# Optimization experiments

Hardware: AMD Instinct MI355X
Metric: run time of the kernel (lower is better)

The kernel has to match this reference:

```python
import jax, jax.numpy as jnp
import numpy as np
from jax.scipy.special import gammaln

REG = 0.1  # reg_param from __init__


def setup_inputs() -> dict:
    key = jax.random.key(0)
    k1, k2 = jax.random.split(key)
    D, C, S, Q = 512, 64, 16, 2048  # feature_dim, n_way, shots, n_query
    X_support = jax.random.normal(k1, (C * S, D), dtype=jnp.float32)
    # balanced class labels (equivalent to argmax of a one-hot y)
    labels = jnp.arange(C * S, dtype=jnp.int32) % C
    X_query = jax.random.normal(k2, (Q, D), dtype=jnp.float32)
    # learned parameters, initialized exactly as in the torch module
    m = jnp.zeros((1, D), dtype=jnp.float32)
    kappa = jnp.asarray(0.1, dtype=jnp.float32)
    nu = jnp.asarray(float(D), dtype=jnp.float32)
    triu_diag = jnp.ones((D,), dtype=jnp.float32)
    triu_lower = jnp.eye(D, dtype=jnp.float32)
    return {"X_support": X_support, "labels": labels, "X_query": X_query,
            "m": m, "kappa": kappa, "nu": nu,
            "triu_diag": triu_diag, "triu_lower": triu_lower, "n_classes": 64}


def _forward(X_support, X_query, m, kappa, nu, triu_diag, triu_lower, labels, n_classes):
    N, D = X_support.shape
    C = int(n_classes)
    S = N // C  # balanced episode: N_j == S for every class

    # lower_triu = diag(|triu_diag|) + triu_lower * strictly_lower_mask
    mask = jnp.tril(jnp.ones((D, D), dtype=X_support.dtype), -1)
    L = jnp.diag(jnp.abs(triu_diag)) + triu_lower * mask

    kap = jnp.abs(kappa) + 1e-6
    nu_ = jnp.clip(nu, D - 1 + 1e-6)

    # group support samples by class: [C, S, D] (stable sort keeps per-class order)
    order = jnp.argsort(labels)
    Xg = X_support[order].reshape(C, S, D)
    Xmean = Xg.mean(axis=1)  # [C, D]

    # posterior means mu_j = kappa/(kappa+N) m + N/(kappa+N) mean(X_j)
    mu = (kap / (kap + S)) * m + (S / (kap + S)) * Xmean  # [C, D]

    # sum_outer(X_j) as one batched GEMM instead of a per-row loop
    XtX = jnp.einsum('csd,cse->cde', Xg, Xg)  # [C, D, D]
    base = L @ L.T + kap * (m.T @ m)          # [D, D], shared across classes
    S_ns = base[None] + XtX - (kap + S) * jnp.einsum('cd,ce->cde', mu, mu)
    sigma = S_ns * ((kap + S + 1.0) / ((nu_ + S - D + 1.0) * (kap + S)))  # [C, D, D]

    eye = jnp.eye(D, dtype=sigma.dtype)
    sigma_inv = (1.0 - REG) * jnp.linalg.inv(sigma) + REG * eye  # regularize()

    common = nu_ + S + 1.0 - D  # scalar (equal shots per class)
    _, logdet = jnp.linalg.slogdet(sigma)  # [C]
    bias = (gammaln(0.5 * (common + D)) - gammaln(0.5 * common)
            - 0.5 * D * jnp.log(common) - 0.5 * logdet)  # [C]

    # batched Mahalanobis distances: replaces nested python loops in predict()
    diff = X_query[None, :, :] - mu[:, None, :]              # [C, Q, D]
    t = jnp.einsum('cqd,cde->cqe', diff, sigma_inv)          # [C, Q, D]
    dist = jnp.sum(t * diff, axis=-1)                        # [C, Q]

    logits = bias[:, None] - 0.5 * (common + D) * jnp.log1p(dist / common)
    return logits.T  # [Q, C]


def reference(X_support, labels, X_query, m, kappa, nu, triu_diag, triu_lower, n_classes):
    return _forward(X_support, X_query, m, kappa, nu, triu_diag, triu_lower,
                    labels, n_classes)
```

## Files before the change

kernel.cpp:

```cpp
#include <hip/hip_runtime.h>
#include <math.h>

#define DD    512
#define CNUM  64
#define SHOTS 16
#define NSUP  1024
#define QNQ   2048
#define REGP  0.1f
#define XKS   4

typedef __attribute__((ext_vector_type(8))) short short8;
typedef __attribute__((ext_vector_type(4))) float f32x4;

__device__ __forceinline__ unsigned short f2bf(float f) {
  unsigned int u = __float_as_uint(f);
  unsigned int r = (u + 0x7fffu + ((u >> 16) & 1u)) >> 16;
  return (unsigned short)r;
}
__device__ __forceinline__ float bf2f(unsigned short h) {
  return __uint_as_float((unsigned int)h << 16);
}

static constexpr size_t OFF_W     = 0;
static constexpr size_t OFF_MU    = OFF_W     + 512*512;
static constexpr size_t OFF_Y     = OFF_MU    + 64*512;
static constexpr size_t OFF_Z     = OFF_Y     + 3136*512;
static constexpr size_t OFF_WM    = OFF_Z     + 3136;
static constexpr size_t OFF_CONST = OFF_WM    + 512;
static constexpr size_t OFF_IDX   = OFF_CONST + 16;
static constexpr size_t OFF_RMAP  = OFF_IDX   + 1024;
static constexpr size_t OFF_ZG    = OFF_RMAP  + 1088;
static constexpr size_t OFF_VMU   = OFF_ZG    + 1088;
static constexpr size_t OFF_MUBMU = OFF_VMU   + 1088;
static constexpr size_t OFF_MUN   = OFF_MUBMU + 64;
static constexpr size_t OFF_MINV  = OFF_MUN   + 64;
static constexpr size_t OFF_BIAS  = OFF_MINV  + 64*289;
static constexpr size_t OFF_QNRM  = OFF_BIAS  + 64;
static constexpr size_t OFF_YN    = OFF_QNRM  + 2048;
static constexpr size_t OFF_XMU   = OFF_YN    + 2048;
static constexpr size_t OFF_RG    = OFF_XMU   + (size_t)XKS*2048*64;
static constexpr size_t OFF_P     = OFF_RG    + 1088*2048;
static constexpr size_t OFF_PX    = OFF_P     + 3136*512;
static constexpr size_t OFF_PW    = OFF_PX    + 3136*512;


__device__ __forceinline__ void px_rows(const float* __restrict__ Xq,
    const float* __restrict__ Xs, unsigned short* __restrict__ PX, int r0) {
  int tid = threadIdx.x;
  int row = r0 + (tid >> 6), lane = tid & 63;
  const float* src = (row < QNQ) ? Xq + (size_t)row * DD
                                 : Xs + (size_t)(row - QNQ) * DD;
  size_t prow = (size_t)row * 1024;
  #pragma unroll
  for (int p = 0; p < 2; p++) {
    int col = lane * 8 + p * 4;
    float4 v = *(const float4*)(src + col);
    ushort4 hi, lo;
    hi.x = f2bf(v.x); lo.x = f2bf(v.x - bf2f(hi.x));
    hi.y = f2bf(v.y); lo.y = f2bf(v.y - bf2f(hi.y));
    hi.z = f2bf(v.z); lo.z = f2bf(v.z - bf2f(hi.z));
    hi.w = f2bf(v.w); lo.w = f2bf(v.w - bf2f(hi.w));
    *(ushort4*)(PX + prow + col) = hi;
    *(ushort4*)(PX + prow + 512 + col) = lo;
  }
}

__global__ __launch_bounds__(256) void f_init(const float* tdiag, const float* tlow,
    const float* kappa, const float* nu, const int* labels, const float* Xs,
    const float* Xq, const float* m, float* W, float* cst, int* idx,
    int* rowmap, float* mu, float* mun,
    unsigned short* PX, unsigned short* PW) {
  __shared__ float sh[2 * 64 * 68 + 32 * 33];
  __shared__ int sidx[SHOTS];
  int b = blockIdx.x, tid = threadIdx.x;
  if (b < 8) {
    int jb = b;
    float* Ld = sh;
    float* Wd = sh + 64 * 68;
    float* tsh = sh + 2 * 64 * 68;
    for (int t = tid; t < 4096; t += 256) {
      int r = t >> 6, c = t & 63;
      int gr = jb * 64 + r;
      float v = (r == c) ? fabsf(tdiag[gr])
              : (r > c ? tlow[(size_t)gr * DD + jb * 64 + c] : 0.0f);
      Ld[r * 68 + c] = v;
      Wd[r * 68 + c] = 0.0f;
    }
    __syncthreads();
    if (tid < 64) {
      int s = tid >> 4, t = tid & 15;
      int r0 = s * 16;
      #pragma unroll
      for (int i = 0; i < 16; i++) {
        float w = (i == t) ? 1.0f : 0.0f;
        #pragma unroll
        for (int k = 0; k < 16; k++)
          if (k < i) w -= Ld[(r0 + i) * 68 + r0 + k] * Wd[(r0 + k) * 68 + r0 + t];
        Wd[(r0 + i) * 68 + r0 + t] = w / Ld[(r0 + i) * 68 + r0 + i];
      }
    }
    __syncthreads();
    for (int g2 = 0; g2 < 2; g2++) {
      int r0 = g2 * 32 + 16, c0 = g2 * 32;
      int rr = tid >> 4, cc = tid & 15;
      float t_ = 0.0f;
      #pragma unroll
      for (int k = 0; k < 16; k++)
        t_ += Ld[(r0 + rr) * 68 + c0 + k] * Wd[(c0 + k) * 68 + c0 + cc];
      tsh[rr * 33 + cc] = t_;
      __syncthreads();
      float x = 0.0f;
      #pragma unroll
      for (int k = 0; k < 16; k++)
        x -= Wd[(r0 + rr) * 68 + r0 + k] * tsh[k * 33 + cc];
      Wd[(r0 + rr) * 68 + c0 + cc] = x;
      __syncthreads();
    }
    {
      int rr = tid >> 6, cc = tid & 63;
      #pragma unroll
      for (int p = 0; p < 4; p++) {
        int r = rr + p * 4, c = cc;
        if (c < 32) {
          float t_ = 0.0f;
          #pragma unroll
          for (int k = 0; k < 32; k++)
            t_ += Ld[(32 + r) * 68 + k] * Wd[k * 68 + c];
          tsh[r * 33 + c] = t_;
        } else {
          int c2 = c - 32;
          float t_ = 0.0f;
          #pragma unroll
          for (int k = 0; k < 32; k++)
            t_ += Ld[(32 + r + 16) * 68 + k] * Wd[k * 68 + c2];
          tsh[(r + 16) * 33 + c2] = t_;
        }
      }
      __syncthreads();
      #pragma unroll
      for (int p = 0; p < 4; p++) {
        int r = rr + p * 4, c = cc;
        int r2 = (c < 32) ? r : r + 16;
        int c2 = (c < 32) ? c : c - 32;
        float x = 0.0f;
        #pragma unroll
        for (int k = 0; k < 32; k++)
          x -= Wd[(32 + r2) * 68 + 32 + k] * tsh[k * 33 + c2];
        Wd[(32 + r2) * 68 + c2] = x;
      }
    }
    __syncthreads();
    float* Wblk = W + (size_t)(jb * 64) * DD + jb * 64;
    for (int t = tid; t < 4096; t += 256) {
      int r = t >> 6, c = t & 63;
      float v = Wd[r * 68 + c];
      Wblk[(size_t)r * DD + c] = v;
      unsigned short h = f2bf(v), l = f2bf(v - bf2f(h));
      size_t prow = (size_t)(jb * 64 + r) * 1024 + jb * 64 + c;
      PW[prow] = h;
      PW[prow + 512] = l;
    }
  } else if (b == 8) {
    if (tid == 0) {
      float kap = fabsf(kappa[0]) + 1e-6f;
      float nu_ = fmaxf(nu[0], (float)(DD - 1) + 1e-6f);
      float common = nu_ + (float)SHOTS + 1.0f - (float)DD;
      float scale = (kap + SHOTS + 1.0f) / ((nu_ + SHOTS - DD + 1.0f) * (kap + SHOTS));
      cst[0] = kap;
      cst[1] = scale;
      cst[2] = common;
      cst[3] = 0.5f * (common + DD);
      cst[4] = lgammaf(0.5f * (common + DD)) - lgammaf(0.5f * common)
               - 0.5f * (float)DD * logf(common);
      cst[5] = -(kap + SHOTS);
      cst[6] = kap / (kap + SHOTS);
      cst[7] = 1.0f / (kap + SHOTS);
      cst[8] = (float)DD * logf(scale);
      cst[9] = -1.0f / (kap + SHOTS);
    }
  } else if (b < 73) {
    int c = b - 9;
    if (tid < 64) {
      int lane = tid, cnt = 0;
      for (int i0 = 0; i0 < NSUP; i0 += 64) {
        int lab = labels[i0 + lane];
        unsigned long long mm = __ballot(lab == c);
        if (lab == c) {
          int pos = cnt + __popcll(mm & ((1ull << lane) - 1ull));
          if (pos < SHOTS) idx[c * SHOTS + pos] = i0 + lane;
        }
        cnt += __popcll(mm);
      }
    }
    __syncthreads();
    if (tid < 17)
      rowmap[c * 17 + tid] = (tid < SHOTS) ? (QNQ + idx[c * SHOTS + tid])
                                           : (QNQ + NSUP + c);
  } else {
    int c = b - 73;
    if (tid < 64) {
      int lane = tid, cnt = 0;
      for (int i0 = 0; i0 < NSUP; i0 += 64) {
        int lab = labels[i0 + lane];
        unsigned long long mm = __ballot(lab == c);
        if (lab == c) {
          int pos = cnt + __popcll(mm & ((1ull << lane) - 1ull));
          if (pos < SHOTS) sidx[pos] = i0 + lane;
        }
        cnt += __popcll(mm);
      }
    }
    __syncthreads();
    float kap = fabsf(kappa[0]) + 1e-6f;
    float cm = kap / (kap + SHOTS), cx = 1.0f / (kap + SHOTS);
    float* red = sh;
    float acc = 0.0f;
    size_t prow = (size_t)(3072 + c) * 1024;
    for (int d = tid; d < DD; d += 256) {
      float s = 0.0f;
      for (int sh_ = 0; sh_ < SHOTS; sh_++)
        s += Xs[(size_t)sidx[sh_] * DD + d];
      float v = cm * m[d] + cx * s;
      mu[(size_t)c * DD + d] = v;
      unsigned short h = f2bf(v), l = f2bf(v - bf2f(h));
      PX[prow + d] = h;
      PX[prow + 512 + d] = l;
      acc += v * v;
    }
    red[tid] = acc;
    __syncthreads();
    for (int off = 128; off > 0; off >>= 1) {
      if (tid < off) red[tid] += red[tid + off];
      __syncthreads();
    }
    if (tid == 0) mun[c] = red[0];
  }
}

__device__ __forceinline__ void tile_stage(float* S, const float* __restrict__ G, int ldg) {
  int tid = threadIdx.x;
  #pragma unroll
  for (int p = 0; p < 4; p++) {
    int f4 = tid + 256 * p;
    int row = f4 >> 4, c4 = (f4 & 15) * 4;
    *(float4*)&S[row * 68 + c4] = *(const float4*)(G + (size_t)row * ldg + c4);
  }
}
__device__ __forceinline__ void tile_fma(float acc[4][4], const float* As, const float* Bs) {
  int tid = threadIdx.x, tr = tid >> 4, tc = tid & 15;
  #pragma unroll
  for (int kk = 0; kk < 64; kk++) {
    float a[4];
    #pragma unroll
    for (int x = 0; x < 4; x++) a[x] = As[(tr * 4 + x) * 68 + kk];
    float4 bv = *(const float4*)&Bs[kk * 68 + tc * 4];
    float bb[4] = {bv.x, bv.y, bv.z, bv.w};
    #pragma unroll
    for (int x = 0; x < 4; x++)
      #pragma unroll
      for (int y = 0; y < 4; y++) acc[x][y] += a[x] * bb[y];
  }
}
__device__ __forceinline__ void tile_out_neg(const float acc[4][4], float* W,
    unsigned short* PW, int gr0, int gc0) {
  int tid = threadIdx.x, tr = tid >> 4, tc = tid & 15;
  #pragma unroll
  for (int x = 0; x < 4; x++) {
    #pragma unroll
    for (int y = 0; y < 4; y++) {
      float v = -acc[x][y];
      W[(size_t)(gr0 + tr * 4 + x) * DD + gc0 + tc * 4 + y] = v;
      unsigned short h = f2bf(v), l = f2bf(v - bf2f(h));
      size_t prow = (size_t)(gr0 + tr * 4 + x) * 1024 + gc0 + tc * 4 + y;
      PW[prow] = h;
      PW[prow + 512] = l;
    }
  }
}

#define GBK 16
__global__ __launch_bounds__(256) void k_m128_xmu(const float* __restrict__ tlow,
    const float* __restrict__ W_, float* __restrict__ Wout,
    const float* __restrict__ Xq, const float* __restrict__ Mu,
    float* __restrict__ xmup, unsigned short* __restrict__ PW) {
  __shared__ float sh[3 * 64 * 68];
  int b = blockIdx.x, tid = threadIdx.x;
  if (b < 4) {
    float* As = sh;
    float* Bs = sh + 64 * 68;
    float* tsh = sh + 2 * 64 * 68;
    int base = b * 128;
    float tacc[4][4] = {};
    tile_stage(As, tlow + (size_t)(base + 64) * DD + base, DD);
    tile_stage(Bs, W_ + (size_t)base * DD + base, DD);
    __syncthreads();
    tile_fma(tacc, As, Bs);
    __syncthreads();
    {
      int tr = tid >> 4, tc = tid & 15;
      #pragma unroll
      for (int x = 0; x < 4; x++)
        #pragma unroll
        for (int y = 0; y < 4; y++) tsh[(tr * 4 + x) * 68 + tc * 4 + y] = tacc[x][y];
    }
    tile_stage(As, W_ + (size_t)(base + 64) * DD + base + 64, DD);
    __syncthreads();
    float xacc[4][4] = {};
    tile_fma(xacc, As, tsh);
    tile_out_neg(xacc, Wout, PW, base + 64, base);
  } else {
    float* Ms = sh;
    float* Qs = sh + 64 * 68;
    int xb = b - 4;
    int bm = (xb & 63) * 32, kq = xb >> 6;
    int tr = tid >> 4, tc = tid & 15;
    float acc[4][2] = {};
    int k0s = kq * (DD / XKS), k0e = k0s + DD / XKS;
    for (int k0 = k0s; k0 < k0e; k0 += GBK) {
      {
        int row = tid >> 2, k4 = tid & 3;
        float4 v = *(const float4*)(Mu + (size_t)row * DD + k0 + k4 * 4);
        Ms[(k4 * 4 + 0) * 68 + row] = v.x; Ms[(k4 * 4 + 1) * 68 + row] = v.y;
        Ms[(k4 * 4 + 2) * 68 + row] = v.z; Ms[(k4 * 4 + 3) * 68 + row] = v.w;
      }
      if (tid < 128) {
        int row = tid >> 2, k4 = tid & 3;
        float4 v = *(const float4*)(Xq + (size_t)(bm + row) * DD + k0 + k4 * 4);
        Qs[(k4 * 4 + 0) * 36 + row] = v.x; Qs[(k4 * 4 + 1) * 36 + row] = v.y;
        Qs[(k4 * 4 + 2) * 36 + row] = v.z; Qs[(k4 * 4 + 3) * 36 + row] = v.w;
      }
      __syncthreads();
      #pragma unroll
      for (int kk = 0; kk < GBK; kk++) {
        float4 m0 = *(const float4*)&Ms[kk * 68 + tr * 4];
        float a[4] = {m0.x, m0.y, m0.z, m0.w};
        float q0 = Qs[kk * 36 + tc * 2], q1 = Qs[kk * 36 + tc * 2 + 1];
        #pragma unroll
        for (int y = 0; y < 4; y++) {
          acc[y][0] += a[y] * q0;
          acc[y][1] += a[y] * q1;
        }
      }
      __syncthreads();
    }
    #pragma unroll
    for (int y = 0; y < 4; y++) {
      float2 v = make_float2(acc[y][0], acc[y][1]);
      *(float2*)(xmup + ((size_t)kq * CNUM + tr * 4 + y) * QNQ + bm + tc * 2) = v;
    }
  }
}

__global__ __launch_bounds__(256) void k_m256(const float* __restrict__ tlow,
    float* __restrict__ W, unsigned short* __restrict__ PW,
    const float* __restrict__ Xq, const float* __restrict__ Xs,
    unsigned short* __restrict__ PX) {
  __shared__ float sh[3 * 64 * 68];
  int b = blockIdx.x, tid = threadIdx.x;
  if (b >= 8) { px_rows(Xq, Xs, PX, (b - 8) * 4); return; }
  float* As = sh;
  float* Bs = sh + 64 * 68;
  float* tsh = sh + 2 * 64 * 68;
  int g = b >> 2, rem = b & 3, i = rem >> 1, j = rem & 1;
  int base = g * 256;
  float xacc[4][4] = {};
  for (int k = 0; k <= i; k++) {
    float tacc[4][4] = {};
    for (int l = j; l < 2; l++) {
      __syncthreads();
      tile_stage(As, tlow + (size_t)(base + 128 + 64 * k) * DD + base + 64 * l, DD);
      tile_stage(Bs, W + (size_t)(base + 64 * l) * DD + base + 64 * j, DD);
      __syncthreads();
      tile_fma(tacc, As, Bs);
    }
    __syncthreads();
    {
      int tr = tid >> 4, tc = tid & 15;
      #pragma unroll
      for (int x = 0; x < 4; x++)
        #pragma unroll
        for (int y = 0; y < 4; y++) tsh[(tr * 4 + x) * 68 + tc * 4 + y] = tacc[x][y];
    }
    tile_stage(As, W + (size_t)(base + 128 + 64 * i) * DD + base + 128 + 64 * k, DD);
    __syncthreads();
    tile_fma(xacc, As, tsh);
  }
  tile_out_neg(xacc, W, PW, base + 128 + 64 * i, base + 64 * j);
}

__device__ __forceinline__ void nn64_sh(float* As, float* Bs,
    const float* __restrict__ A, int lda, const float* __restrict__ B, int ldb,
    float* __restrict__ Cd, int ldc, int k0, int k1, float sgn,
    unsigned short* __restrict__ Pw, int gr0, int gc0) {
  int tid = threadIdx.x, tr = tid >> 4, tc = tid & 15;
  float acc[4][4] = {};
  for (int kc = k0; kc < k1; kc += 64) {
    #pragma unroll
    for (int p = 0; p < 4; p++) {
      int f4 = tid + 256 * p;
      int row = f4 >> 4, c4 = f4 & 15;
      *(float4*)&As[row * 68 + c4 * 4] = *(const float4*)(A + (size_t)row * lda + kc + c4 * 4);
      *(float4*)&Bs[row * 68 + c4 * 4] = *(const float4*)(B + (size_t)(kc + row) * ldb + c4 * 4);
    }
    __syncthreads();
    #pragma unroll
    for (int kk = 0; kk < 64; kk++) {
      float a[4];
      #pragma unroll
      for (int x = 0; x < 4; x++) a[x] = As[(tr * 4 + x) * 68 + kk];
      float4 bv = *(const float4*)&Bs[kk * 68 + tc * 4];
      float bb[4] = {bv.x, bv.y, bv.z, bv.w};
      #pragma unroll
      for (int x = 0; x < 4; x++)
        #pragma unroll
        for (int y = 0; y < 4; y++) acc[x][y] += a[x] * bb[y];
    }
    __syncthreads();
  }
  #pragma unroll
  for (int x = 0; x < 4; x++) {
    float4 v = make_float4(sgn * acc[x][0], sgn * acc[x][1],
                           sgn * acc[x][2], sgn * acc[x][3]);
    *(float4*)(Cd + (size_t)(tr * 4 + x) * ldc + tc * 4) = v;
    if (Pw) {
      size_t prow = (size_t)(gr0 + tr * 4 + x) * 1024 + gc0 + tc * 4;
      float vv[4] = {v.x, v.y, v.z, v.w};
      #pragma unroll
      for (int y = 0; y < 4; y++) {
        unsigned short h = f2bf(vv[y]), l = f2bf(vv[y] - bf2f(h));
        Pw[prow + y] = h;
        Pw[prow + 512 + y] = l;
      }
    }
  }
}

__global__ __launch_bounds__(256) void k_triT(const float* __restrict__ tlow,
                                              const float* __restrict__ W,
                                              float* __restrict__ T,
                                              const float* __restrict__ Xq,
                                              const float* __restrict__ Xs,
                                              unsigned short* __restrict__ PX) {
  __shared__ float sh[2 * 64 * 68];
  int b = blockIdx.x;
  if (b >= 16) { px_rows(Xq, Xs, PX, 1024 + (b - 16) * 4); return; }
  int ti = b >> 2, tj = b & 3;
  const float* A = tlow + (size_t)(256 + ti * 64) * DD;
  const float* B = W + (size_t)tj * 64;
  float* Cd = T + (size_t)(ti * 64) * 256 + tj * 64;
  nn64_sh(sh, sh + 64 * 68, A, DD, B, DD, Cd, 256, tj * 64, 256, 1.0f, nullptr, 0, 0);
}

__global__ __launch_bounds__(256) void k_triX(float* __restrict__ W,
                                              const float* __restrict__ T,
                                              unsigned short* __restrict__ PW,
                                              const float* __restrict__ Xq,
                                              const float* __restrict__ Xs,
                                              unsigned short* __restrict__ PX) {
  __shared__ float sh[2 * 64 * 68];
  int b = blockIdx.x;
  if (b >= 16) { px_rows(Xq, Xs, PX, 2048 + (b - 16) * 4); return; }
  int ti = b >> 2, tj = b & 3;
  const float* A = W + (size_t)(256 + ti * 64) * DD + 256;
  const float* B = T + tj * 64;
  int gr0 = 256 + ti * 64, gc0 = tj * 64;
  float* Cd = W + (size_t)gr0 * DD + gc0;
  nn64_sh(sh, sh + 64 * 68, A, DD, B, 256, Cd, DD, 0, (ti + 1) * 64, -1.0f, PW, gr0, gc0);
}

#define PSTR 72
__global__ __launch_bounds__(256) void f_y_wm(const unsigned short* __restrict__ PX,
    const unsigned short* __restrict__ PW, const float* __restrict__ W,
    const float* __restrict__ m, float* __restrict__ Y,
    unsigned short* __restrict__ Pm, float* __restrict__ wm) {
  __shared__ unsigned short AshH[64 * PSTR];
  __shared__ unsigned short AshL[64 * PSTR];
  __shared__ unsigned short BshH[64 * PSTR];
  __shared__ unsigned short BshL[64 * PSTR];
  int b = blockIdx.x, tid = threadIdx.x;
  if (b < 392) {
    int mt = b >> 3, nt = b & 7;
    int bm = mt * 64, bn = nt * 64;
    int lane = tid & 63, wave = tid >> 6;
    int wr = wave >> 1, wc = wave & 1;
    int mrow = lane & 15, q = lane >> 4;
    f32x4 acc00 = {}, acc01 = {}, acc10 = {}, acc11 = {};
    int kchunks = nt + 1;
    for (int it = 0; it < kchunks; it++) {
      int kc = it * 64;
      #pragma unroll
      for (int p = 0; p < 2; p++) {
        int idx = tid + 256 * p;
        int row = idx >> 3, c8 = (idx & 7) * 8;
        *(short8*)&AshH[row * PSTR + c8] =
            *(const short8*)(PX + (size_t)(bm + row) * 1024 + kc + c8);
        *(short8*)&AshL[row * PSTR + c8] =
            *(const short8*)(PX + (size_t)(bm + row) * 1024 + 512 + kc + c8);
        *(short8*)&BshH[row * PSTR + c8] =
            *(const short8*)(PW + (size_t)(bn + row) * 1024 + kc + c8);
        *(short8*)&BshL[row * PSTR + c8] =
            *(const short8*)(PW + (size_t)(bn + row) * 1024 + 512 + kc + c8);
      }
      __syncthreads();
      #pragma unroll
      for (int ks = 0; ks < 2; ks++) {
        int ko = ks * 32 + q * 8;
        short8 ah0 = *(const short8*)&AshH[(wr * 32 + mrow) * PSTR + ko];
        short8 ah1 = *(const short8*)&AshH[(wr * 32 + 16 + mrow) * PSTR + ko];
        short8 al0 = *(const short8*)&AshL[(wr * 32 + mrow) * PSTR + ko];
        short8 al1 = *(const short8*)&AshL[(wr * 32 + 16 + mrow) * PSTR + ko];
        short8 bh0 = *(const short8*)&BshH[(wc * 32 + mrow) * PSTR + ko];
        short8 bh1 = *(const short8*)&BshH[(wc * 32 + 16 + mrow) * PSTR + ko];
        short8 bl0 = *(const short8*)&BshL[(wc * 32 + mrow) * PSTR + ko];
        short8 bl1 = *(const short8*)&BshL[(wc * 32 + 16 + mrow) * PSTR + ko];
        acc00 = __builtin_amdgcn_mfma_f32_16x16x32_bf16(ah0, bh0, acc00, 0, 0, 0);
        acc00 = __builtin_amdgcn_mfma_f32_16x16x32_bf16(ah0, bl0, acc00, 0, 0, 0);
        acc00 = __builtin_amdgcn_mfma_f32_16x16x32_bf16(al0, bh0, acc00, 0, 0, 0);
        acc01 = __builtin_amdgcn_mfma_f32_16x16x32_bf16(ah0, bh1, acc01, 0, 0, 0);
        acc01 = __builtin_amdgcn_mfma_f32_16x16x32_bf16(ah0, bl1, acc01, 0, 0, 0);
        acc01 = __builtin_amdgcn_mfma_f32_16x16x32_bf16(al0, bh1, acc01, 0, 0, 0);
        acc10 = __builtin_amdgcn_mfma_f32_16x16x32_bf16(ah1, bh0, acc10, 0, 0, 0);
        acc10 = __builtin_amdgcn_mfma_f32_16x16x32_bf16(ah1, bl0, acc10, 0, 0, 0);
        acc10 = __builtin_amdgcn_mfma_f32_16x16x32_bf16(al1, bh0, acc10, 0, 0, 0);
        acc11 = __builtin_amdgcn_mfma_f32_16x16x32_bf16(ah1, bh1, acc11, 0, 0, 0);
        acc11 = __builtin_amdgcn_mfma_f32_16x16x32_bf16(ah1, bl1, acc11, 0, 0, 0);
        acc11 = __builtin_amdgcn_mfma_f32_16x16x32_bf16(al1, bh1, acc11, 0, 0, 0);
      }
      __syncthreads();
    }
    #pragma unroll
    for (int r = 0; r < 4; r++) {
      int row0 = bm + wr * 32 + q * 4 + r;
      int row1 = row0 + 16;
      int col0 = bn + wc * 32 + mrow;
      float vv[4] = {acc00[r], acc01[r], acc10[r], acc11[r]};
      int rows[4] = {row0, row0, row1, row1};
      int cols[4] = {col0, col0 + 16, col0, col0 + 16};
      #pragma unroll
      for (int e = 0; e < 4; e++) {
        Y[(size_t)rows[e] * DD + cols[e]] = vv[e];
        unsigned short h = f2bf(vv[e]), l = f2bf(vv[e] - bf2f(h));
        Pm[(size_t)rows[e] * 1024 + cols[e]] = h;
        Pm[(size_t)rows[e] * 1024 + 512 + cols[e]] = l;
      }
    }
  } else {
    int wave = tid >> 6, lane = tid & 63;
    int row = (b - 392) * 4 + wave;
    float s = 0.0f;
    for (int j = lane; j <= row; j += 64) s += W[(size_t)row * DD + j] * m[j];
    for (int off = 32; off > 0; off >>= 1) s += __shfl_down(s, off);
    if (lane == 0) wm[row] = s;
  }
}

__global__ __launch_bounds__(256) void f_z_rg_gram(const unsigned short* __restrict__ Pm,
    const float* __restrict__ Y, const float* __restrict__ tdiag,
    const int* __restrict__ rowmap, const float* __restrict__ Xq,
    const float* __restrict__ wm, float* __restrict__ cst,
    float* __restrict__ Rg,
    float* __restrict__ z, float* __restrict__ qn, float* __restrict__ yn,
    float* __restrict__ zg, float* __restrict__ Vmu, float* __restrict__ muBmu,
    float* __restrict__ Minv, float* __restrict__ bias) {
  __shared__ float sh[9216];
  __shared__ float csmS;
  int b = blockIdx.x, tid = threadIdx.x;
  if (b < 64) {
    int c = b;
    int lane = tid & 63, wave = tid >> 6;
    float* Ys  = sh;
    float* aug = sh + 8772;
    float* zsv = aug + 306;
    float kap = cst[0], cst9 = cst[9];
    for (int t = tid; t < 17 * 128; t += 256) {
      int r = t >> 7, col = t & 127;
      *(float4*)&Ys[r * 516 + col * 4] =
          *(const float4*)(Y + (size_t)rowmap[c * 17 + r] * DD + col * 4);
    }
    float ldb_r = 0.0f;
    if (wave == 0) {
      float aa = 0.0f, ll = 0.0f;
      for (int t = lane; t < DD; t += 64) {
        float w = wm[t]; aa += w * w;
        ll += logf(fabsf(tdiag[t]));
      }
      #pragma unroll
      for (int off = 32; off > 0; off >>= 1) {
        aa += __shfl_xor(aa, off);
        ll += __shfl_xor(ll, off);
      }
      ldb_r = 2.0f * ll + logf(1.0f + kap * aa);
      if (lane == 0) csmS = kap / (1.0f + kap * aa);
    }
    __syncthreads();
    if (wave > 0) {
      for (int a = wave - 1; a < 17; a += 3) {
        float s = 0.0f;
        for (int j = lane; j < 128; j += 64) {
          float4 yv = *(const float4*)&Ys[a * 516 + j * 4];
          float4 wv = *(const float4*)(wm + j * 4);
          s += yv.x * wv.x + yv.y * wv.y + yv.z * wv.z + yv.w * wv.w;
        }
        #pragma unroll
        for (int off = 32; off > 0; off >>= 1) s += __shfl_xor(s, off);
        if (lane == 0) zsv[a] = s;
      }
    }
    __syncthreads();
    float csm = csmS;
    for (int e = tid; e < 153; e += 256) {
      int a = (int)((sqrtf(8.0f * (float)e + 1.0f) - 1.0f) * 0.5f);
      while (((a + 1) * (a + 2)) / 2 <= e) a++;
      while ((a * (a + 1)) / 2 > e) a--;
      int bb = e - (a * (a + 1)) / 2;
      const float* ra = &Ys[a * 516];
      const float* rb = &Ys[bb * 516];
      float s = 0.0f;
      for (int k = 0; k < 128; k++) {
        float4 va = *(const float4*)&ra[k * 4];
        float4 vb = *(const float4*)&rb[k * 4];
        s += va.x * vb.x + va.y * vb.y + va.z * vb.z + va.w * vb.w;
      }
      float g = s - csm * zsv[a] * zsv[bb];
      if (a == bb) g += (a < 16) ? 1.0f : cst9;
      aug[a * 18 + bb] = g;
      if (a != bb) aug[bb * 18 + a] = g;
    }
    __syncthreads();
    if (wave == 0) {
      float colv[17];
      bool left = lane < 17;
      bool right = (lane >= 17 && lane < 34);
      #pragma unroll
      for (int r = 0; r < 17; r++) {
        float lv = aug[r * 18 + (lane & 31)];
        colv[r] = left ? lv : ((right && (lane - 17) == r) ? 1.0f : 0.0f);
      }
      float det = 0.0f;
      #pragma unroll
      for (int k = 0; k < 17; k++) {
        float best = fabsf(colv[k]); int bp = k;
        #pragma unroll
        for (int r = k + 1; r < 17; r++) {
          float v = fabsf(colv[r]);
          if (v > best) { best = v; bp = r; }
        }
        int p = __shfl(bp, k);
        float pv = colv[k];
        #pragma unroll
        for (int r = k + 1; r < 17; r++) pv = (p == r) ? colv[r] : pv;
        float oldk = colv[k];
        #pragma unroll
        for (int r = k + 1; r < 17; r++) colv[r] = (p == r) ? oldk : colv[r];
        colv[k] = pv;
        float piv = __shfl(pv, k);
        if (lane == 0) det += logf(fabsf(piv));
        float invp = 1.0f / piv;
        float rk = pv * invp;
        colv[k] = rk;
        #pragma unroll
        for (int r = 0; r < 17; r++) {
          if (r == k) continue;
          float ck = __shfl(colv[r], k);
          colv[r] = fmaf(-ck, rk, colv[r]);
        }
      }
      if (right) {
        int bb = lane - 17;
        #pragma unroll
        for (int r = 0; r < 17; r++)
          Minv[(size_t)c * 289 + r * 17 + bb] = colv[r];
      }
      if (lane == 0) {
        float slog = logf(fabsf(cst[5])) + det;
        float logdetSigma = cst[8] + ldb_r + slog;
        bias[c] = cst[4] - 0.5f * logdetSigma;
      }
    } else if (wave == 1) {
      if (lane < 17) {
        float gv = aug[lane * 18 + 16];
        if (lane == 16) gv -= cst9;
        Vmu[c * 17 + lane] = gv;
        if (lane == 16) muBmu[c] = gv;
        zg[c * 17 + lane] = zsv[lane];
      }
    }
  } else if (b == 64) {
    if (tid < 64) {
      float aa = 0.0f, ll = 0.0f;
      for (int t = tid; t < DD; t += 64) {
        float w = wm[t]; aa += w * w;
        ll += logf(fabsf(tdiag[t]));
      }
      #pragma unroll
      for (int off = 32; off > 0; off >>= 1) {
        aa += __shfl_xor(aa, off);
        ll += __shfl_xor(ll, off);
      }
      if (tid == 0) {
        float kap = cst[0];
        cst[10] = kap / (1.0f + kap * aa);
        cst[11] = 2.0f * ll + logf(1.0f + kap * aa);
      }
    }
  } else if (b < 609) {
    unsigned short* ush = (unsigned short*)sh;
    unsigned short* AH = ush;
    unsigned short* AL = ush + 64 * PSTR;
    unsigned short* BH = ush + 2 * 64 * PSTR;
    unsigned short* BL = ush + 3 * 64 * PSTR;
    int rb = b - 65;
    int bm = (rb >> 5) * 64, bn = (rb & 31) * 64;
    int lane = tid & 63, wave = tid >> 6;
    int wr = wave >> 1, wc = wave & 1;
    int mrow = lane & 15, q = lane >> 4;
    int srowA[2];
    #pragma unroll
    for (int p = 0; p < 2; p++) srowA[p] = rowmap[bm + ((tid + 256 * p) >> 3)];
    f32x4 acc00 = {}, acc01 = {}, acc10 = {}, acc11 = {};
    for (int it = 0; it < 8; it++) {
      int kc = it * 64;
      #pragma unroll
      for (int p = 0; p < 2; p++) {
        int idx = tid + 256 * p;
        int row = idx >> 3, c8 = (idx & 7) * 8;
        *(short8*)&AH[row * PSTR + c8] =
            *(const short8*)(Pm + (size_t)srowA[p] * 1024 + kc + c8);
        *(short8*)&AL[row * PSTR + c8] =
            *(const short8*)(Pm + (size_t)srowA[p] * 1024 + 512 + kc + c8);
        *(short8*)&BH[row * PSTR + c8] =
            *(const short8*)(Pm + (size_t)(bn + row) * 1024 + kc + c8);
        *(short8*)&BL[row * PSTR + c8] =
            *(const short8*)(Pm + (size_t)(bn + row) * 1024 + 512 + kc + c8);
      }
      __syncthreads();
      #pragma unroll
      for (int ks = 0; ks < 2; ks++) {
        int ko = ks * 32 + q * 8;
        short8 ah0 = *(const short8*)&AH[(wr * 32 + mrow) * PSTR + ko];
        short8 ah1 = *(const short8*)&AH[(wr * 32 + 16 + mrow) * PSTR + ko];
        short8 al0 = *(const short8*)&AL[(wr * 32 + mrow) * PSTR + ko];
        short8 al1 = *(const short8*)&AL[(wr * 32 + 16 + mrow) * PSTR + ko];
        short8 bh0 = *(const short8*)&BH[(wc * 32 + mrow) * PSTR + ko];
        short8 bh1 = *(const short8*)&BH[(wc * 32 + 16 + mrow) * PSTR + ko];
        short8 bl0 = *(const short8*)&BL[(wc * 32 + mrow) * PSTR + ko];
        short8 bl1 = *(const short8*)&BL[(wc * 32 + 16 + mrow) * PSTR + ko];
        acc00 = __builtin_amdgcn_mfma_f32_16x16x32_bf16(ah0, bh0, acc00, 0, 0, 0);
        acc00 = __builtin_amdgcn_mfma_f32_16x16x32_bf16(ah0, bl0, acc00, 0, 0, 0);
        acc00 = __builtin_amdgcn_mfma_f32_16x16x32_bf16(al0, bh0, acc00, 0, 0, 0);
        acc01 = __builtin_amdgcn_mfma_f32_16x16x32_bf16(ah0, bh1, acc01, 0, 0, 0);
        acc01 = __builtin_amdgcn_mfma_f32_16x16x32_bf16(ah0, bl1, acc01, 0, 0, 0);
        acc01 = __builtin_amdgcn_mfma_f32_16x16x32_bf16(al0, bh1, acc01, 0, 0, 0);
        acc10 = __builtin_amdgcn_mfma_f32_16x16x32_bf16(ah1, bh0, acc10, 0, 0, 0);
        acc10 = __builtin_amdgcn_mfma_f32_16x16x32_bf16(ah1, bl0, acc10, 0, 0, 0);
        acc10 = __builtin_amdgcn_mfma_f32_16x16x32_bf16(al1, bh0, acc10, 0, 0, 0);
        acc11 = __builtin_amdgcn_mfma_f32_16x16x32_bf16(ah1, bh1, acc11, 0, 0, 0);
        acc11 = __builtin_amdgcn_mfma_f32_16x16x32_bf16(ah1, bl1, acc11, 0, 0, 0);
        acc11 = __builtin_amdgcn_mfma_f32_16x16x32_bf16(al1, bh1, acc11, 0, 0, 0);
      }
      __syncthreads();
    }
    #pragma unroll
    for (int r = 0; r < 4; r++) {
      int row0 = bm + wr * 32 + q * 4 + r;
      int row1 = row0 + 16;
      int col0 = bn + wc * 32 + mrow;
      Rg[(size_t)row0 * QNQ + col0]      = acc00[r];
      Rg[(size_t)row0 * QNQ + col0 + 16] = acc01[r];
      Rg[(size_t)row1 * QNQ + col0]      = acc10[r];
      Rg[(size_t)row1 * QNQ + col0 + 16] = acc11[r];
    }
  } else {
    int wave = tid >> 6, lane = tid & 63;
    int row = (b - 609) * 4 + wave;
    const float* xr = Xq + (size_t)row * DD;
    const float* yr = Y + (size_t)row * DD;
    float sz = 0.0f, s1 = 0.0f, s2 = 0.0f;
    for (int j4 = lane; j4 < 128; j4 += 64) {
      float4 xv = *(const float4*)(xr + j4 * 4);
      float4 yv = *(const float4*)(yr + j4 * 4);
      float4 wv = *(const float4*)(wm + j4 * 4);
      sz += yv.x * wv.x + yv.y * wv.y + yv.z * wv.z + yv.w * wv.w;
      s1 += xv.x * xv.x + xv.y * xv.y + xv.z * xv.z + xv.w * xv.w;
      s2 += yv.x * yv.x + yv.y * yv.y + yv.z * yv.z + yv.w * yv.w;
    }
    for (int off = 32; off > 0; off >>= 1) {
      sz += __shfl_down(sz, off);
      s1 += __shfl_down(s1, off);
      s2 += __shfl_down(s2, off);
    }
    if (lane == 0) {
      z[row] = sz;
      qn[row] = s1;
      yn[row] = s2;
    }
  }
}

__global__ __launch_bounds__(256) void k_logits(const float* __restrict__ Rg,
    const float* z, const float* zg,
    const float* Vmu, const float* muBmu, const float* mun, const float* yn,
    const float* qn, const float* xmup, const float* Minv, const float* bias,
    const float* cst, float* out) {
  __shared__ float Ms[289], Vs[17], Zs[17];
  int c = blockIdx.y;
  int q = blockIdx.x * 256 + threadIdx.x;
  for (int t = threadIdx.x; t < 289; t += 256) Ms[t] = Minv[(size_t)c * 289 + t];
  if (threadIdx.x < 17) {
    Vs[threadIdx.x] = Vmu[c * 17 + threadIdx.x];
    Zs[threadIdx.x] = zg[c * 17 + threadIdx.x];
  }
  __syncthreads();
  float csm = cst[10], scale = cst[1], common = cst[2], coef = cst[3];
  float zq = z[q];
  float r[17];
  float xBmu = 0.0f;
  for (int a = 0; a < 17; a++) {
    float raw = Rg[(size_t)(c * 17 + a) * QNQ + q] - csm * Zs[a] * zq;
    if (a == 16) xBmu = raw;
    r[a] = raw - Vs[a];
  }
  float qB = yn[q] - csm * zq * zq;
  float quadB = qB - 2.0f * xBmu + muBmu[c];
  float corr = 0.0f;
  for (int a = 0; a < 17; a++) {
    float e = 0.0f;
    for (int bb = 0; bb < 17; bb++) e += Ms[a * 17 + bb] * r[bb];
    corr += r[a] * e;
  }
  float distB = (quadB - corr) / scale;
  float xm = 0.0f;
  #pragma unroll
  for (int p = 0; p < XKS; p++)
    xm += xmup[((size_t)(p * CNUM + c)) * QNQ + q];
  float dn = qn[q] - 2.0f * xm + mun[c];
  float dist = (1.0f - REGP) * distB + REGP * dn;
  out[(size_t)q * CNUM + c] = bias[c] - coef * log1pf(dist / common);
}

extern "C" void kernel_launch(void* const* d_in, const int* in_sizes, int n_in,
                              void* d_out, int out_size, void* d_ws, size_t ws_size,
                              hipStream_t stream) {
  const float* Xs    = (const float*)d_in[0];
  const int*   labels= (const int*)d_in[1];
  const float* Xq    = (const float*)d_in[2];
  const float* m     = (const float*)d_in[3];
  const float* kappa = (const float*)d_in[4];
  const float* nu    = (const float*)d_in[5];
  const float* tdiag = (const float*)d_in[6];
  const float* tlow  = (const float*)d_in[7];
  float* ws = (float*)d_ws;
  float* W    = ws + OFF_W;
  float* mu   = ws + OFF_MU;
  float* Y    = ws + OFF_Y;
  float* z    = ws + OFF_Z;
  float* wm   = ws + OFF_WM;
  float* cst  = ws + OFF_CONST;
  int*   idx  = (int*)(ws + OFF_IDX);
  int*   rmap = (int*)(ws + OFF_RMAP);
  float* zg   = ws + OFF_ZG;
  float* Vmu  = ws + OFF_VMU;
  float* muBmu= ws + OFF_MUBMU;
  float* mun  = ws + OFF_MUN;
  float* Minv = ws + OFF_MINV;
  float* bias = ws + OFF_BIAS;
  float* qn   = ws + OFF_QNRM;
  float* yn   = ws + OFF_YN;
  float* xmup = ws + OFF_XMU;
  float* Rg   = ws + OFF_RG;
  unsigned short* P  = (unsigned short*)(ws + OFF_P);
  unsigned short* PX = (unsigned short*)(ws + OFF_PX);
  unsigned short* PW = (unsigned short*)(ws + OFF_PW);
  float* Ttmp = ws + OFF_RG;
  float* out  = (float*)d_out;

  f_init<<<137, 256, 0, stream>>>(tdiag, tlow, kappa, nu, labels, Xs, Xq, m,
                                  W, cst, idx, rmap, mu, mun, PX, PW);
  k_m128_xmu<<<260, 256, 0, stream>>>(tlow, W, W, Xq, mu, xmup, PW);
  k_m256<<<8 + 256, 256, 0, stream>>>(tlow, W, PW, Xq, Xs, PX);
  k_triT<<<16 + 256, 256, 0, stream>>>(tlow, W, Ttmp, Xq, Xs, PX);
  k_triX<<<16 + 256, 256, 0, stream>>>(W, Ttmp, PW, Xq, Xs, PX);
  f_y_wm<<<520, 256, 0, stream>>>(PX, PW, W, m, Y, P, wm);
  f_z_rg_gram<<<64 + 1 + 544 + 512, 256, 0, stream>>>(P, Y, tdiag, rmap, Xq, wm,
                                                      cst, Rg, z, qn, yn,
                                                      zg, Vmu, muBmu, Minv, bias);
  k_logits<<<dim3(QNQ / 256, CNUM), 256, 0, stream>>>(Rg, z, zg, Vmu, muBmu,
                                                      mun, yn, qn, xmup, Minv, bias,
                                                      cst, out);
  (void)in_sizes; (void)n_in; (void)out_size; (void)ws_size;
}
```

Baseline: 187.5 us.

## Merge label-index blocks, keep triangular inverse in registers, widen k-tile, batch rows

The rowmap computation moves into the mu blocks, which drops 64 redundant f_init blocks and the idx workspace buffer. The 16x16 diagonal-block triangular inverse now keeps its running column in registers instead of re-reading shared memory. The k_m128_xmu k-step doubles to 32 so each tile loads twice as much and there are fewer loop iterations and barriers. The row-norm blocks of f_z_rg_gram now handle two rows per wave, which halves their block count.

```diff
diff --git a/kernel.cpp b/kernel.cpp
--- a/kernel.cpp
+++ b/kernel.cpp
@@ -27,8 +27,7 @@
 static constexpr size_t OFF_Z     = OFF_Y     + 3136*512;
 static constexpr size_t OFF_WM    = OFF_Z     + 3136;
 static constexpr size_t OFF_CONST = OFF_WM    + 512;
-static constexpr size_t OFF_IDX   = OFF_CONST + 16;
-static constexpr size_t OFF_RMAP  = OFF_IDX   + 1024;
+static constexpr size_t OFF_RMAP  = OFF_CONST + 16;
 static constexpr size_t OFF_ZG    = OFF_RMAP  + 1088;
 static constexpr size_t OFF_VMU   = OFF_ZG    + 1088;
 static constexpr size_t OFF_MUBMU = OFF_VMU   + 1088;
@@ -67,7 +66,7 @@
 
 __global__ __launch_bounds__(256) void f_init(const float* tdiag, const float* tlow,
     const float* kappa, const float* nu, const int* labels, const float* Xs,
-    const float* Xq, const float* m, float* W, float* cst, int* idx,
+    const float* Xq, const float* m, float* W, float* cst,
     int* rowmap, float* mu, float* mun,
     unsigned short* PX, unsigned short* PW) {
   __shared__ float sh[2 * 64 * 68 + 32 * 33];
@@ -90,14 +89,17 @@
     if (tid < 64) {
       int s = tid >> 4, t = tid & 15;
       int r0 = s * 16;
+      float wreg[16];
       #pragma unroll
       for (int i = 0; i < 16; i++) {
         float w = (i == t) ? 1.0f : 0.0f;
         #pragma unroll
         for (int k = 0; k < 16; k++)
-          if (k < i) w -= Ld[(r0 + i) * 68 + r0 + k] * Wd[(r0 + k) * 68 + r0 + t];
-        Wd[(r0 + i) * 68 + r0 + t] = w / Ld[(r0 + i) * 68 + r0 + i];
-      }
+          if (k < i) w -= Ld[(r0 + i) * 68 + r0 + k] * wreg[k];
+        wreg[i] = w / Ld[(r0 + i) * 68 + r0 + i];
+      }
+      #pragma unroll
+      for (int i = 0; i < 16; i++) Wd[(r0 + i) * 68 + r0 + t] = wreg[i];
     }
     __syncthreads();
     for (int g2 = 0; g2 < 2; g2++) {
@@ -178,26 +180,8 @@
       cst[8] = (float)DD * logf(scale);
       cst[9] = -1.0f / (kap + SHOTS);
     }
-  } else if (b < 73) {
+  } else {
     int c = b - 9;
-    if (tid < 64) {
-      int lane = tid, cnt = 0;
-      for (int i0 = 0; i0 < NSUP; i0 += 64) {
-        int lab = labels[i0 + lane];
-        unsigned long long mm = __ballot(lab == c);
-        if (lab == c) {
-          int pos = cnt + __popcll(mm & ((1ull << lane) - 1ull));
-          if (pos < SHOTS) idx[c * SHOTS + pos] = i0 + lane;
-        }
-        cnt += __popcll(mm);
-      }
-    }
-    __syncthreads();
-    if (tid < 17)
-      rowmap[c * 17 + tid] = (tid < SHOTS) ? (QNQ + idx[c * SHOTS + tid])
-                                           : (QNQ + NSUP + c);
-  } else {
-    int c = b - 73;
     if (tid < 64) {
       int lane = tid, cnt = 0;
       for (int i0 = 0; i0 < NSUP; i0 += 64) {
@@ -211,6 +195,8 @@
       }
     }
     __syncthreads();
+    if (tid < 17)
+      rowmap[c * 17 + tid] = (tid < SHOTS) ? (QNQ + sidx[tid]) : (QNQ + NSUP + c);
     float kap = fabsf(kappa[0]) + 1e-6f;
     float cm = kap / (kap + SHOTS), cx = 1.0f / (kap + SHOTS);
     float* red = sh;
@@ -278,7 +264,7 @@
   }
 }
 
-#define GBK 16
+#define GBK 32
 __global__ __launch_bounds__(256) void k_m128_xmu(const float* __restrict__ tlow,
     const float* __restrict__ W_, float* __restrict__ Wout,
     const float* __restrict__ Xq, const float* __restrict__ Mu,
@@ -317,14 +303,16 @@
     float acc[4][2] = {};
     int k0s = kq * (DD / XKS), k0e = k0s + DD / XKS;
     for (int k0 = k0s; k0 < k0e; k0 += GBK) {
-      {
-        int row = tid >> 2, k4 = tid & 3;
+      #pragma unroll
+      for (int p = 0; p < 2; p++) {
+        int idx = tid + 256 * p;
+        int row = idx >> 3, k4 = idx & 7;
         float4 v = *(const float4*)(Mu + (size_t)row * DD + k0 + k4 * 4);
         Ms[(k4 * 4 + 0) * 68 + row] = v.x; Ms[(k4 * 4 + 1) * 68 + row] = v.y;
         Ms[(k4 * 4 + 2) * 68 + row] = v.z; Ms[(k4 * 4 + 3) * 68 + row] = v.w;
       }
-      if (tid < 128) {
-        int row = tid >> 2, k4 = tid & 3;
+      {
+        int row = tid >> 3, k4 = tid & 7;
         float4 v = *(const float4*)(Xq + (size_t)(bm + row) * DD + k0 + k4 * 4);
         Qs[(k4 * 4 + 0) * 36 + row] = v.x; Qs[(k4 * 4 + 1) * 36 + row] = v.y;
         Qs[(k4 * 4 + 2) * 36 + row] = v.z; Qs[(k4 * 4 + 3) * 36 + row] = v.w;
@@ -772,27 +760,31 @@
     }
   } else {
     int wave = tid >> 6, lane = tid & 63;
-    int row = (b - 609) * 4 + wave;
-    const float* xr = Xq + (size_t)row * DD;
-    const float* yr = Y + (size_t)row * DD;
-    float sz = 0.0f, s1 = 0.0f, s2 = 0.0f;
-    for (int j4 = lane; j4 < 128; j4 += 64) {
-      float4 xv = *(const float4*)(xr + j4 * 4);
-      float4 yv = *(const float4*)(yr + j4 * 4);
-      float4 wv = *(const float4*)(wm + j4 * 4);
-      sz += yv.x * wv.x + yv.y * wv.y + yv.z * wv.z + yv.w * wv.w;
-      s1 += xv.x * xv.x + xv.y * xv.y + xv.z * xv.z + xv.w * xv.w;
-      s2 += yv.x * yv.x + yv.y * yv.y + yv.z * yv.z + yv.w * yv.w;
-    }
-    for (int off = 32; off > 0; off >>= 1) {
-      sz += __shfl_down(sz, off);
-      s1 += __shfl_down(s1, off);
-      s2 += __shfl_down(s2, off);
-    }
-    if (lane == 0) {
-      z[row] = sz;
-      qn[row] = s1;
-      yn[row] = s2;
+    int base = (b - 609) * 8;
+    #pragma unroll
+    for (int rr = 0; rr < 2; rr++) {
+      int row = base + rr * 4 + wave;
+      const float* xr = Xq + (size_t)row * DD;
+      const float* yr = Y + (size_t)row * DD;
+      float sz = 0.0f, s1 = 0.0f, s2 = 0.0f;
+      for (int j4 = lane; j4 < 128; j4 += 64) {
+        float4 xv = *(const float4*)(xr + j4 * 4);
+        float4 yv = *(const float4*)(yr + j4 * 4);
+        float4 wv = *(const float4*)(wm + j4 * 4);
+        sz += yv.x * wv.x + yv.y * wv.y + yv.z * wv.z + yv.w * wv.w;
+        s1 += xv.x * xv.x + xv.y * xv.y + xv.z * xv.z + xv.w * xv.w;
+        s2 += yv.x * yv.x + yv.y * yv.y + yv.z * yv.z + yv.w * yv.w;
+      }
+      for (int off = 32; off > 0; off >>= 1) {
+        sz += __shfl_down(sz, off);
+        s1 += __shfl_down(s1, off);
+        s2 += __shfl_down(s2, off);
+      }
+      if (lane == 0) {
+        z[row] = sz;
+        qn[row] = s1;
+        yn[row] = s2;
+      }
     }
   }
 }
@@ -856,7 +848,6 @@
   float* z    = ws + OFF_Z;
   float* wm   = ws + OFF_WM;
   float* cst  = ws + OFF_CONST;
-  int*   idx  = (int*)(ws + OFF_IDX);
   int*   rmap = (int*)(ws + OFF_RMAP);
   float* zg   = ws + OFF_ZG;
   float* Vmu  = ws + OFF_VMU;
@@ -874,14 +865,14 @@
   float* Ttmp = ws + OFF_RG;
   float* out  = (float*)d_out;
 
-  f_init<<<137, 256, 0, stream>>>(tdiag, tlow, kappa, nu, labels, Xs, Xq, m,
-                                  W, cst, idx, rmap, mu, mun, PX, PW);
+  f_init<<<73, 256, 0, stream>>>(tdiag, tlow, kappa, nu, labels, Xs, Xq, m,
+                                 W, cst, rmap, mu, mun, PX, PW);
   k_m128_xmu<<<260, 256, 0, stream>>>(tlow, W, W, Xq, mu, xmup, PW);
   k_m256<<<8 + 256, 256, 0, stream>>>(tlow, W, PW, Xq, Xs, PX);
   k_triT<<<16 + 256, 256, 0, stream>>>(tlow, W, Ttmp, Xq, Xs, PX);
   k_triX<<<16 + 256, 256, 0, stream>>>(W, Ttmp, PW, Xq, Xs, PX);
   f_y_wm<<<520, 256, 0, stream>>>(PX, PW, W, m, Y, P, wm);
-  f_z_rg_gram<<<64 + 1 + 544 + 512, 256, 0, stream>>>(P, Y, tdiag, rmap, Xq, wm,
+  f_z_rg_gram<<<64 + 1 + 544 + 256, 256, 0, stream>>>(P, Y, tdiag, rmap, Xq, wm,
                                                       cst, Rg, z, qn, yn,
                                                       zg, Vmu, muBmu, Minv, bias);
   k_logits<<<dim3(QNQ / 256, CNUM), 256, 0, stream>>>(Rg, z, zg, Vmu, muBmu,
```

Measured after the change: 186.8 us. No clear change (-0.4%).
